# Kernel optimization log

Measured on AMD Instinct MI355X. Metric: run time of the kernel, lower is better.

## Reference

```python
import jax, jax.numpy as jnp
import numpy as np

B, S, D, F, E, K, H = 4, 1024, 512, 2048, 8, 2, 8
HEAD_DIM = D // H


def setup_inputs() -> dict:
    key = jax.random.key(0)
    ks = jax.random.split(key, 8)
    s = 0.02
    return {
        "x": jax.random.normal(ks[0], (B, S, D), jnp.float32),
        "gate_Wk": jax.random.normal(ks[1], (D, D), jnp.float32) * s,
        "gate_bk": jnp.zeros((D,), jnp.float32),
        "expert_queries": jax.random.normal(ks[2], (E, D), jnp.float32),
        "Wqkv": jax.random.normal(ks[3], (E, 3 * D, D), jnp.float32) * s,
        "bqkv": jnp.zeros((E, 3 * D), jnp.float32),
        "Wo": jax.random.normal(ks[4], (E, D, D), jnp.float32) * s,
        "bo": jnp.zeros((E, D), jnp.float32),
        "g1": jnp.ones((E, D), jnp.float32),
        "be1": jnp.zeros((E, D), jnp.float32),
        "W1": jax.random.normal(ks[5], (E, F, D), jnp.float32) * s,
        "bf1": jnp.zeros((E, F), jnp.float32),
        "W2": jax.random.normal(ks[6], (E, D, F), jnp.float32) * s,
        "bf2": jnp.zeros((E, D), jnp.float32),
        "g2": jnp.ones((E, D), jnp.float32),
        "be2": jnp.zeros((E, D), jnp.float32),
    }


def _layernorm(x, g, b):
    m = x.mean(-1, keepdims=True)
    v = ((x - m) ** 2).mean(-1, keepdims=True)
    return (x - m) * jax.lax.rsqrt(v + 1e-5) * g + b


def _expert(x, Wqkv, bqkv, Wo, bo, g1, be1, W1, bf1, W2, bf2, g2, be2):
    # x: [B,S,D]; one ExpertTransformerDecoder block (dropout=0, eval)
    b, s, d = x.shape
    qkv = x @ Wqkv.T + bqkv                      # [B,S,3D]
    q, k, v = jnp.split(qkv, 3, axis=-1)
    to_heads = lambda t: t.reshape(b, s, H, HEAD_DIM).transpose(0, 2, 1, 3)
    q, k, v = to_heads(q), to_heads(k), to_heads(v)
    scale = 1.0 / np.sqrt(HEAD_DIM).astype(np.float32)
    attn = jax.nn.softmax(jnp.einsum('bhqd,bhkd->bhqk', q * scale, k), axis=-1)
    ctx = jnp.einsum('bhqk,bhkd->bhqd', attn, v).transpose(0, 2, 1, 3).reshape(b, s, d)
    ctx = ctx @ Wo.T + bo
    x = _layernorm(x + ctx, g1, be1)
    h = jax.nn.gelu(x @ W1.T + bf1, approximate=False)
    h = jax.nn.gelu(h @ W2.T + bf2, approximate=False)
    return _layernorm(x + h, g2, be2)


def reference(x, gate_Wk, gate_bk, expert_queries, Wqkv, bqkv, Wo, bo,
              g1, be1, W1, bf1, W2, bf2, g2, be2):
    # attention gating: softmax over experts of <key_proj(x), expert_q> * d^-0.5
    keys = x @ gate_Wk.T + gate_bk                      # [B,S,D]
    scores = jnp.einsum('bsd,ed->bse', keys, expert_queries) * (D ** -0.5)
    probs = jax.nn.softmax(scores, axis=-1)             # [B,S,E]
    # top-k mask + renormalize
    _, idx = jax.lax.top_k(probs, K)                    # [B,S,K]
    mask = jax.nn.one_hot(idx, E, dtype=probs.dtype).sum(-2)
    gated = probs * mask
    gated = gated / (gated.sum(-1, keepdims=True) + 1e-9)
    # run all experts densely (as the torch code does), vmapped over E
    eo = jax.vmap(_expert, in_axes=(None,) + (0,) * 12)(
        x, Wqkv, bqkv, Wo, bo, g1, be1, W1, bf1, W2, bf2, g2, be2)  # [E,B,S,D]
    return jnp.einsum('ebsd,bse->bsd', eo, gated)
```

## Files before the change

### kernel.cpp

```cpp
#include <hip/hip_runtime.h>
#include <cstdint>
#include <cmath>

#define Bc 4
#define Sc 1024
#define Dc 512
#define Fc 2048
#define Ec 8
#define Hc 8
#define Mc 4096

typedef unsigned short u16;
typedef __attribute__((ext_vector_type(8))) short bf16x8;
typedef __attribute__((ext_vector_type(4))) float f32x4;

__device__ __forceinline__ float bf2f(u16 u) {
  unsigned v = ((unsigned)u) << 16;
  return __builtin_bit_cast(float, v);
}
__device__ __forceinline__ u16 f2bf(float f) {
  unsigned u = __builtin_bit_cast(unsigned, f);
  unsigned r = 0x7fffu + ((u >> 16) & 1u);
  return (u16)((u + r) >> 16);
}
__device__ __forceinline__ unsigned pack2bf(float a, float b) {
  return (unsigned)f2bf(a) | ((unsigned)f2bf(b) << 16);
}
__device__ __forceinline__ float gelu_f(float x) {
  const float z = 1.5957691216057308f * fmaf(0.044715f * x, x * x, x);
  const float e = __expf(z);
  return x * (1.0f - __builtin_amdgcn_rcpf(e + 1.0f));
}
__device__ __forceinline__ void async16(const void* g, void* l) {
  __builtin_amdgcn_global_load_lds(
      (const __attribute__((address_space(1))) unsigned int*)g,
      (__attribute__((address_space(3))) unsigned int*)l, 16, 0, 0);
}

__global__ __launch_bounds__(256) void cvt_kernel(const float* __restrict__ in,
                                                  u16* __restrict__ outp, long long n) {
  const long long i = ((long long)blockIdx.x * 256 + threadIdx.x) * 4;
  if (i < n) {
    const float4 v = *(const float4*)(in + i);
    ushort4 o;
    o.x = f2bf(v.x); o.y = f2bf(v.y); o.z = f2bf(v.z); o.w = f2bf(v.w);
    *(ushort4*)(outp + i) = o;
  }
}

__global__ __launch_bounds__(256) void weq_kernel(const float* __restrict__ gWk,
                                                  const float* __restrict__ eq,
                                                  float* __restrict__ weq) {
  __shared__ float red[4][64];
  const int tid = threadIdx.x, wave = tid >> 6, lane = tid & 63;
  const int d = blockIdx.x * 64 + lane;
  const int e = blockIdx.y;
  float acc = 0.f;
  for (int j = wave * 128; j < wave * 128 + 128; ++j)
    acc += gWk[(long long)j * 512 + d] * eq[e * 512 + j];
  red[wave][lane] = acc;
  __syncthreads();
  if (wave == 0)
    weq[e * 512 + d] = red[0][lane] + red[1][lane] + red[2][lane] + red[3][lane];
}
__global__ void beq_kernel(const float* __restrict__ gbk, const float* __restrict__ eq,
                           float* __restrict__ beq) {
  const int wave = threadIdx.x >> 6, lane = threadIdx.x & 63;
  for (int e = wave; e < 8; e += 4) {
    float a = 0.f;
#pragma unroll
    for (int i = 0; i < 8; ++i) a += gbk[lane + 64 * i] * eq[e * 512 + lane + 64 * i];
#pragma unroll
    for (int off = 32; off; off >>= 1) a += __shfl_xor(a, off);
    if (lane == 0) beq[e] = a;
  }
}

__global__ __launch_bounds__(256) void gate_kernel(const float* __restrict__ x,
                                                   const float* __restrict__ weq,
                                                   const float* __restrict__ beq,
                                                   float* __restrict__ gated,
                                                   int* __restrict__ cnt, int* __restrict__ tlist,
                                                   int* __restrict__ pos) {
  const int wave = threadIdx.x >> 6, lane = threadIdx.x & 63;
  const int t = blockIdx.x * 4 + wave;
  const float* xr = x + (long long)t * 512;
  float acc[8] = {};
#pragma unroll
  for (int i = 0; i < 8; ++i) {
    const float xv = xr[lane + 64 * i];
#pragma unroll
    for (int e2 = 0; e2 < 8; ++e2) acc[e2] += xv * weq[e2 * 512 + lane + 64 * i];
  }
#pragma unroll
  for (int e2 = 0; e2 < 8; ++e2)
#pragma unroll
    for (int off = 32; off; off >>= 1) acc[e2] += __shfl_xor(acc[e2], off);
  if (lane == 0) {
    const float scale = 0.044194173824159216f;
    float s[8], mx = -1e30f;
#pragma unroll
    for (int e2 = 0; e2 < 8; ++e2) { s[e2] = (acc[e2] + beq[e2]) * scale; mx = fmaxf(mx, s[e2]); }
    float p[8], sum = 0.f;
#pragma unroll
    for (int e2 = 0; e2 < 8; ++e2) { p[e2] = expf(s[e2] - mx); sum += p[e2]; }
#pragma unroll
    for (int e2 = 0; e2 < 8; ++e2) p[e2] /= sum;
    int i1 = 0;
#pragma unroll
    for (int e2 = 1; e2 < 8; ++e2) if (p[e2] > p[i1]) i1 = e2;
    int i2 = (i1 == 0) ? 1 : 0;
#pragma unroll
    for (int e2 = 0; e2 < 8; ++e2) if (e2 != i1 && e2 != i2 && p[e2] > p[i2]) i2 = e2;
    const float denom = p[i1] + p[i2] + 1e-9f;
#pragma unroll
    for (int e2 = 0; e2 < 8; ++e2)
      gated[t * 8 + e2] = (e2 == i1 || e2 == i2) ? p[e2] / denom : 0.f;
    const int b = t >> 10;
    int s1 = atomicAdd(cnt + i1 * 4 + b, 1);
    tlist[(i1 * 4 + b) * 1024 + s1] = t;
    pos[i1 * 4096 + t] = s1;
    int s2 = atomicAdd(cnt + i2 * 4 + b, 1);
    tlist[(i2 * 4 + b) * 1024 + s2] = t;
    pos[i2 * 4096 + t] = s2;
  }
}

__global__ void pad_kernel(const int* __restrict__ cnt, int* __restrict__ tlist) {
  const int seg = blockIdx.x;
  const int c = cnt[seg];
  const int ce = (c + 127) & ~127;
  const int tpad = (seg & 3) << 10;
  for (int i = c + (int)threadIdx.x; i < ce; i += 128) tlist[seg * 1024 + i] = tpad;
}

__global__ void wl_kernel(const int* __restrict__ cnt, int* __restrict__ wl) {
  const int seg = threadIdx.x;
  if (seg >= 32) return;
  int base = 0;
  for (int s = 0; s < seg; ++s) base += (cnt[s] + 127) >> 7;
  const int nt = (cnt[seg] + 127) >> 7;
  for (int t = 0; t < nt; ++t) wl[base + t] = (seg << 8) | t;
  for (int t = 0; t < 2 * nt; ++t) wl[128 + 2 * base + t] = (seg << 8) | t;
  if (seg == 31) { wl[96] = base + nt; wl[97] = 2 * (base + nt); }
}

template <int GELU, int QKV, int ROUTED, int BK>
__global__ __launch_bounds__(256) void gemm_bf16(
    const u16* __restrict__ A, const u16* __restrict__ Bw, const float* __restrict__ bias,
    u16* __restrict__ Cout, u16* __restrict__ vT, int M, int N, int K, long long Astride,
    const int* __restrict__ wl) {
  int e;
  long long bm;
  if (ROUTED) {
    const int total = wl[96];
    if ((int)blockIdx.x >= total) return;
    const int item = wl[blockIdx.x];
    const int seg = item >> 8, tile = item & 255;
    e = seg >> 2;
    bm = ((long long)(seg & 3) << 10) + tile * 128;
  } else {
    e = blockIdx.z;
    bm = (long long)blockIdx.x * 128;
  }
  __shared__ __attribute__((aligned(16))) u16 As[128 * BK];
  __shared__ __attribute__((aligned(16))) u16 Bs[128 * BK];
  const int tid = threadIdx.x;
  const int wave = tid >> 6, lane = tid & 63;
  const long long bn = (long long)blockIdx.y * 128;
  const u16* Ag = A + (long long)e * Astride + bm * K;
  const u16* Bg = Bw + ((long long)e * N + bn) * K;
  constexpr int LPR = BK / 8;
  constexpr int RPI = 512 / BK;
  constexpr int IPW = BK / 16;
  const int lrow = lane / LPR, lpos = lane % LPR;
  const int lm = lane & 15, quad = lane >> 4;
  const int wm = (wave >> 1) * 64, wn = (wave & 1) * 64;
  f32x4 acc[4][4] = {};
  for (int kk = 0; kk < K; kk += BK) {
    __syncthreads();
#pragma unroll
    for (int i = 0; i < IPW; ++i) {
      const int gi = wave * IPW + i;
      const int row = gi * RPI + lrow;
      const int sc = lpos ^ (row & 7);
      async16(Ag + (long long)row * K + kk + sc * 8, &As[gi * 512]);
      async16(Bg + (long long)row * K + kk + sc * 8, &Bs[gi * 512]);
    }
    __syncthreads();
#pragma unroll
    for (int ks = 0; ks < BK / 32; ++ks) {
      bf16x8 af[4], bfr[4];
#pragma unroll
      for (int mi = 0; mi < 4; ++mi) {
        const int row = wm + mi * 16 + lm;
        const int ch = (ks * 4 + quad) ^ (row & 7);
        af[mi] = *(const bf16x8*)(As + row * BK + ch * 8);
      }
#pragma unroll
      for (int nj = 0; nj < 4; ++nj) {
        const int row = wn + nj * 16 + lm;
        const int ch = (ks * 4 + quad) ^ (row & 7);
        bfr[nj] = *(const bf16x8*)(Bs + row * BK + ch * 8);
      }
#pragma unroll
      for (int mi = 0; mi < 4; ++mi)
#pragma unroll
        for (int nj = 0; nj < 4; ++nj)
          acc[mi][nj] = __builtin_amdgcn_mfma_f32_16x16x32_bf16(bfr[nj], af[mi], acc[mi][nj], 0, 0, 0);
    }
  }
  const float* bs = bias + (long long)e * N;
#pragma unroll
  for (int mi = 0; mi < 4; ++mi) {
    const int m = (int)bm + wm + mi * 16 + lm;
#pragma unroll
    for (int nj = 0; nj < 4; ++nj) {
      const int n0 = (int)bn + wn + nj * 16 + quad * 4;
      const float4 bv = *(const float4*)(bs + n0);
      float v0 = acc[mi][nj][0] + bv.x;
      float v1 = acc[mi][nj][1] + bv.y;
      float v2 = acc[mi][nj][2] + bv.z;
      float v3 = acc[mi][nj][3] + bv.w;
      if (GELU) { v0 = gelu_f(v0); v1 = gelu_f(v1); v2 = gelu_f(v2); v3 = gelu_f(v3); }
      if (QKV) {
        if (n0 < 1024) {
          uint2 pk; pk.x = pack2bf(v0, v1); pk.y = pack2bf(v2, v3);
          *(uint2*)(Cout + ((long long)e * Mc + m) * 1024 + n0) = pk;
        } else {
          const int hh = (n0 - 1024) >> 6, dd = (n0 - 1024) & 63;
          const int bb = m >> 10, ss = m & 1023;
          u16* vp = vT + ((((long long)e * Bc + bb) * Hc + hh) * 64 + dd) * Sc + ss;
          vp[0] = f2bf(v0); vp[Sc] = f2bf(v1); vp[2 * Sc] = f2bf(v2); vp[3 * Sc] = f2bf(v3);
        }
      } else {
        uint2 pk; pk.x = pack2bf(v0, v1); pk.y = pack2bf(v2, v3);
        *(uint2*)(Cout + ((long long)e * M + m) * N + n0) = pk;
      }
    }
  }
}

__global__ __launch_bounds__(256, 4) void attn_tile(const u16* __restrict__ qk,
                                                    const u16* __restrict__ vT,
                                                    u16* __restrict__ ctx,
                                                    const int* __restrict__ wl,
                                                    const int* __restrict__ tlist) {
  if ((int)blockIdx.x >= wl[97]) return;
  const int item = wl[128 + blockIdx.x];
  const int seg = item >> 8, qt = item & 255;
  const int e = seg >> 2, b = seg & 3, h = blockIdx.y;
  __shared__ __attribute__((aligned(16))) u16 Ks[64 * 64];
  __shared__ __attribute__((aligned(16))) u16 Vs[64 * 64];
  __shared__ __attribute__((aligned(16))) u16 Pl[4][16 * 72];
  const int tid = threadIdx.x, wave = tid >> 6, lane = tid & 63;
  const int lm = lane & 15, quad = lane >> 4;
  const u16* qkbase = qk + (long long)e * Mc * 1024;
  const u16* vbase = vT + ((((long long)e * Bc + b) * Hc + h) * 64) * Sc;
  const int lr = lane >> 3, lc = (lane & 7) ^ lr;
  u16* P = &Pl[wave][0];
  unsigned* P32 = (unsigned*)P;
  const int pwbase = lm * 36 + quad * 2;

  const long long pidx = (long long)seg * 1024 + qt * 64 + wave * 16 + lm;
  const int tq = tlist[pidx];
  bf16x8 aq[2];
#pragma unroll
  for (int ks = 0; ks < 2; ++ks)
    aq[ks] = *(const bf16x8*)(qkbase + (long long)tq * 1024 + h * 64 + ks * 32 + quad * 8);
  f32x4 O[4] = {};
  float lsum = 0.f;

  for (int n0 = 0; n0 < Sc; n0 += 64) {
    __syncthreads();
#pragma unroll
    for (int i = 0; i < 2; ++i) {
      const int rg = wave * 2 + i;
      const int row = rg * 8 + lr;
      async16(qkbase + ((long long)b * Sc + n0 + row) * 1024 + 512 + h * 64 + lc * 8,
              &Ks[rg * 512]);
      async16(vbase + (long long)row * Sc + n0 + lc * 8, &Vs[rg * 512]);
    }
    __syncthreads();
    f32x4 sT[4];
#pragma unroll
    for (int kj = 0; kj < 4; ++kj) {
      const int row = kj * 16 + lm;
      const bf16x8 k0 = *(const bf16x8*)(Ks + row * 64 + ((quad) ^ (row & 7)) * 8);
      const bf16x8 k1 = *(const bf16x8*)(Ks + row * 64 + ((4 + quad) ^ (row & 7)) * 8);
      f32x4 c = {};
      c = __builtin_amdgcn_mfma_f32_16x16x32_bf16(k0, aq[0], c, 0, 0, 0);
      c = __builtin_amdgcn_mfma_f32_16x16x32_bf16(k1, aq[1], c, 0, 0, 0);
      sT[kj] = c;
    }
#pragma unroll
    for (int kj = 0; kj < 4; ++kj) {
      const float p0 = __expf(sT[kj][0] * 0.125f);
      const float p1 = __expf(sT[kj][1] * 0.125f);
      const float p2 = __expf(sT[kj][2] * 0.125f);
      const float p3 = __expf(sT[kj][3] * 0.125f);
      lsum += (p0 + p1) + (p2 + p3);
      P32[pwbase + kj * 8 + 0] = pack2bf(p0, p1);
      P32[pwbase + kj * 8 + 1] = pack2bf(p2, p3);
    }
    asm volatile("s_waitcnt lgkmcnt(0)" ::: "memory");
    const bf16x8 ap0 = *(const bf16x8*)(P + lm * 72 + quad * 8);
    const bf16x8 ap1 = *(const bf16x8*)(P + lm * 72 + 32 + quad * 8);
#pragma unroll
    for (int d4 = 0; d4 < 4; ++d4) {
      const int row = d4 * 16 + lm;
      const bf16x8 v0 = *(const bf16x8*)(Vs + row * 64 + ((quad) ^ (row & 7)) * 8);
      const bf16x8 v1 = *(const bf16x8*)(Vs + row * 64 + ((4 + quad) ^ (row & 7)) * 8);
      O[d4] = __builtin_amdgcn_mfma_f32_16x16x32_bf16(v0, ap0, O[d4], 0, 0, 0);
      O[d4] = __builtin_amdgcn_mfma_f32_16x16x32_bf16(v1, ap1, O[d4], 0, 0, 0);
    }
  }
  float ls = lsum;
  ls += __shfl_xor(ls, 16);
  ls += __shfl_xor(ls, 32);
  const float inv = 1.0f / ls;
#pragma unroll
  for (int d4 = 0; d4 < 4; ++d4) {
    uint2 pk;
    pk.x = pack2bf(O[d4][0] * inv, O[d4][1] * inv);
    pk.y = pack2bf(O[d4][2] * inv, O[d4][3] * inv);
    *(uint2*)(ctx + pidx * 512 + h * 64 + d4 * 16 + quad * 4) = pk;
  }
}

__global__ __launch_bounds__(256) void ln1_kernel(const float* __restrict__ x,
                                                  const u16* __restrict__ ctxp,
                                                  const float* __restrict__ g1,
                                                  const float* __restrict__ be1,
                                                  u16* __restrict__ x1,
                                                  const int* __restrict__ cnt,
                                                  const int* __restrict__ tlist) {
  const int i = blockIdx.x, b = blockIdx.y, e = blockIdx.z;
  const int seg = (e << 2) + b;
  const int ce = (cnt[seg] + 127) & ~127;
  if (i >= ce) return;
  const long long p = seg * 1024 + i;
  const int t = tlist[p];
  const int tid = threadIdx.x;
  const int wave = tid >> 6, lane = tid & 63;
  __shared__ float sred[4], qred[4];
  const float v0 = x[(long long)t * 512 + tid] + bf2f(ctxp[p * 512 + tid]);
  const float v1 = x[(long long)t * 512 + tid + 256] + bf2f(ctxp[p * 512 + tid + 256]);
  float s = v0 + v1, q = v0 * v0 + v1 * v1;
#pragma unroll
  for (int off = 32; off; off >>= 1) { s += __shfl_xor(s, off); q += __shfl_xor(q, off); }
  if (lane == 0) { sred[wave] = s; qred[wave] = q; }
  __syncthreads();
  s = sred[0] + sred[1] + sred[2] + sred[3];
  q = qred[0] + qred[1] + qred[2] + qred[3];
  const float mean = s * (1.0f / 512.0f);
  const float var = q * (1.0f / 512.0f) - mean * mean;
  const float rstd = rsqrtf(var + 1e-5f);
  x1[p * 512 + tid] = f2bf((v0 - mean) * rstd * g1[e * 512 + tid] + be1[e * 512 + tid]);
  x1[p * 512 + tid + 256] =
      f2bf((v1 - mean) * rstd * g1[e * 512 + tid + 256] + be1[e * 512 + tid + 256]);
}

__global__ __launch_bounds__(256) void ln2_kernel(const u16* __restrict__ x1,
                                                  const u16* __restrict__ h2,
                                                  const float* __restrict__ g2,
                                                  const float* __restrict__ be2,
                                                  const float* __restrict__ gated,
                                                  const int* __restrict__ pos,
                                                  float* __restrict__ out) {
  const int t = blockIdx.x, tid = threadIdx.x;
  const int b = t >> 10;
  const int wave = tid >> 6, lane = tid & 63;
  __shared__ float sred[4], qred[4];
  float o0 = 0.f, o1 = 0.f;
  for (int e = 0; e < 8; ++e) {
    const float wgt = gated[t * 8 + e];
    if (wgt != 0.f) {
      const long long p = ((e << 2) + b) * 1024 + pos[e * 4096 + t];
      const float v0 = bf2f(x1[p * 512 + tid]) + bf2f(h2[p * 512 + tid]);
      const float v1 = bf2f(x1[p * 512 + tid + 256]) + bf2f(h2[p * 512 + tid + 256]);
      float s = v0 + v1, q = v0 * v0 + v1 * v1;
#pragma unroll
      for (int off = 32; off; off >>= 1) { s += __shfl_xor(s, off); q += __shfl_xor(q, off); }
      if (lane == 0) { sred[wave] = s; qred[wave] = q; }
      __syncthreads();
      s = sred[0] + sred[1] + sred[2] + sred[3];
      q = qred[0] + qred[1] + qred[2] + qred[3];
      __syncthreads();
      const float mean = s * (1.0f / 512.0f);
      const float var = q * (1.0f / 512.0f) - mean * mean;
      const float rstd = rsqrtf(var + 1e-5f);
      o0 += wgt * ((v0 - mean) * rstd * g2[e * 512 + tid] + be2[e * 512 + tid]);
      o1 += wgt * ((v1 - mean) * rstd * g2[e * 512 + tid + 256] + be2[e * 512 + tid + 256]);
    }
  }
  out[(long long)t * 512 + tid] = o0;
  out[(long long)t * 512 + tid + 256] = o1;
}

extern "C" void kernel_launch(void* const* d_in, const int* in_sizes, int n_in, void* d_out,
                              int out_size, void* d_ws, size_t ws_size, hipStream_t stream) {
  const float* x    = (const float*)d_in[0];
  const float* gWk  = (const float*)d_in[1];
  const float* gbk  = (const float*)d_in[2];
  const float* eq   = (const float*)d_in[3];
  const float* Wqkv = (const float*)d_in[4];
  const float* bqkv = (const float*)d_in[5];
  const float* Wo   = (const float*)d_in[6];
  const float* bo   = (const float*)d_in[7];
  const float* g1   = (const float*)d_in[8];
  const float* be1  = (const float*)d_in[9];
  const float* W1   = (const float*)d_in[10];
  const float* bf1  = (const float*)d_in[11];
  const float* W2   = (const float*)d_in[12];
  const float* bf2  = (const float*)d_in[13];
  const float* g2   = (const float*)d_in[14];
  const float* be2  = (const float*)d_in[15];
  float* out = (float*)d_out;

  char* wsp = (char*)d_ws;
  size_t off = 0;
  auto take = [&](size_t bytes) -> void* {
    void* p = wsp + off;
    off += (bytes + 255) & ~(size_t)255;
    return p;
  };
  u16* xb    = (u16*)take((size_t)Mc * 512 * 2);
  u16* Wqkvb = (u16*)take((size_t)Ec * 1536 * 512 * 2);
  u16* Wob   = (u16*)take((size_t)Ec * 512 * 512 * 2);
  u16* W1b   = (u16*)take((size_t)Ec * 2048 * 512 * 2);
  u16* W2b   = (u16*)take((size_t)Ec * 512 * 2048 * 2);
  float* weq   = (float*)take(8 * 512 * 4);
  float* beqb  = (float*)take(8 * 4);
  float* gated = (float*)take((size_t)Mc * 8 * 4);
  int* cnt   = (int*)take(32 * 4);
  int* tlist = (int*)take(32 * 1024 * 4);
  int* pos   = (int*)take((size_t)Ec * Mc * 4);
  int* wl    = (int*)take(512 * 4);
  char* big = (char*)take(134217728);
  u16* qkb  = (u16*)big;
  u16* vTb  = (u16*)(big + 67108864);
  u16* ctxp = (u16*)(big + 100663296);
  u16* hb   = (u16*)big;
  u16* ctxb = (u16*)take(33554432);
  u16* h2b  = ctxb;
  u16* x1b  = (u16*)take(33554432);
  (void)in_sizes; (void)n_in; (void)out_size; (void)ws_size;

  cvt_kernel<<<dim3(2048), dim3(256), 0, stream>>>(x, xb, (long long)Mc * 512);
  cvt_kernel<<<dim3(6144), dim3(256), 0, stream>>>(Wqkv, Wqkvb, (long long)Ec * 1536 * 512);
  cvt_kernel<<<dim3(2048), dim3(256), 0, stream>>>(Wo, Wob, (long long)Ec * 512 * 512);
  cvt_kernel<<<dim3(8192), dim3(256), 0, stream>>>(W1, W1b, (long long)Ec * 2048 * 512);
  cvt_kernel<<<dim3(8192), dim3(256), 0, stream>>>(W2, W2b, (long long)Ec * 512 * 2048);
  hipMemsetAsync(cnt, 0, 32 * 4, stream);
  weq_kernel<<<dim3(8, 8), dim3(256), 0, stream>>>(gWk, eq, weq);
  beq_kernel<<<dim3(1), dim3(256), 0, stream>>>(gbk, eq, beqb);
  gate_kernel<<<dim3(1024), dim3(256), 0, stream>>>(x, weq, beqb, gated, cnt, tlist, pos);
  pad_kernel<<<dim3(32), dim3(128), 0, stream>>>(cnt, tlist);
  wl_kernel<<<dim3(1), dim3(64), 0, stream>>>(cnt, wl);
  gemm_bf16<0, 1, 0, 64><<<dim3(32, 12, 8), dim3(256), 0, stream>>>(xb, Wqkvb, bqkv, qkb, vTb, Mc, 1536, 512, 0LL, wl);
  attn_tile<<<dim3(192, 8), dim3(256), 0, stream>>>(qkb, vTb, ctxb, wl, tlist);
  gemm_bf16<0, 0, 1, 128><<<dim3(96, 4), dim3(256), 0, stream>>>(ctxb, Wob, bo, ctxp, nullptr, Mc, 512, 512, (long long)Mc * 512, wl);
  ln1_kernel<<<dim3(1024, 4, 8), dim3(256), 0, stream>>>(x, ctxp, g1, be1, x1b, cnt, tlist);
  gemm_bf16<1, 0, 1, 128><<<dim3(96, 16), dim3(256), 0, stream>>>(x1b, W1b, bf1, hb, nullptr, Mc, 2048, 512, (long long)Mc * 512, wl);
  gemm_bf16<1, 0, 1, 128><<<dim3(96, 4), dim3(256), 0, stream>>>(hb, W2b, bf2, h2b, nullptr, Mc, 512, 2048, (long long)Mc * 2048, wl);
  ln2_kernel<<<dim3(4096), dim3(256), 0, stream>>>(x1b, h2b, g2, be2, gated, pos, out);
}
```

Measured before the change: 509.7 us.

## Compute Q projection only for routed tokens via gathered GEMM; fuse weight conversions

The dense QKV GEMM now computes only K and V for every token. Q is computed by a separate routed GEMM that gathers A rows through the token list, so it covers only the tokens assigned to each expert. The attention kernel reads Q directly by routed position and reads K from its own buffer, with no tlist indirection. The five fp32-to-bf16 conversion launches are merged into one kernel. The intent is to skip Q projection work for unrouted tokens and to cut launch overhead, at the cost of gathered, less coalesced A loads in the Q GEMM.

```diff
diff --git a/kernel.cpp b/kernel.cpp
--- a/kernel.cpp
+++ b/kernel.cpp
@@ -37,15 +37,24 @@
       (__attribute__((address_space(3))) unsigned int*)l, 16, 0, 0);
 }
 
-__global__ __launch_bounds__(256) void cvt_kernel(const float* __restrict__ in,
-                                                  u16* __restrict__ outp, long long n) {
-  const long long i = ((long long)blockIdx.x * 256 + threadIdx.x) * 4;
-  if (i < n) {
-    const float4 v = *(const float4*)(in + i);
-    ushort4 o;
-    o.x = f2bf(v.x); o.y = f2bf(v.y); o.z = f2bf(v.z); o.w = f2bf(v.w);
-    *(ushort4*)(outp + i) = o;
-  }
+__global__ __launch_bounds__(256) void cvt5_kernel(const float* __restrict__ p0, u16* __restrict__ q0,
+                                                   const float* __restrict__ p1, u16* __restrict__ q1,
+                                                   const float* __restrict__ p2, u16* __restrict__ q2,
+                                                   const float* __restrict__ p3, u16* __restrict__ q3,
+                                                   const float* __restrict__ p4, u16* __restrict__ q4) {
+  int bx = blockIdx.x;
+  const float* in;
+  u16* outp;
+  if (bx < 2048) { in = p0; outp = q0; }
+  else if (bx < 8192) { in = p1; outp = q1; bx -= 2048; }
+  else if (bx < 10240) { in = p2; outp = q2; bx -= 8192; }
+  else if (bx < 18432) { in = p3; outp = q3; bx -= 10240; }
+  else { in = p4; outp = q4; bx -= 18432; }
+  const long long i = ((long long)bx * 256 + threadIdx.x) * 4;
+  const float4 v = *(const float4*)(in + i);
+  ushort4 o;
+  o.x = f2bf(v.x); o.y = f2bf(v.y); o.z = f2bf(v.z); o.w = f2bf(v.w);
+  *(ushort4*)(outp + i) = o;
 }
 
 __global__ __launch_bounds__(256) void weq_kernel(const float* __restrict__ gWk,
@@ -145,11 +154,11 @@
   if (seg == 31) { wl[96] = base + nt; wl[97] = 2 * (base + nt); }
 }
 
-template <int GELU, int QKV, int ROUTED, int BK>
+template <int GELU, int QKV, int ROUTED, int BK, int GATHER>
 __global__ __launch_bounds__(256) void gemm_bf16(
     const u16* __restrict__ A, const u16* __restrict__ Bw, const float* __restrict__ bias,
     u16* __restrict__ Cout, u16* __restrict__ vT, int M, int N, int K, long long Astride,
-    const int* __restrict__ wl) {
+    long long Bstride, const int* __restrict__ wl, const int* __restrict__ tlist) {
   int e;
   long long bm;
   if (ROUTED) {
@@ -169,13 +178,22 @@
   const int wave = tid >> 6, lane = tid & 63;
   const long long bn = (long long)blockIdx.y * 128;
   const u16* Ag = A + (long long)e * Astride + bm * K;
-  const u16* Bg = Bw + ((long long)e * N + bn) * K;
+  const u16* Bg = Bw + ((long long)e * Bstride + bn) * K;
   constexpr int LPR = BK / 8;
   constexpr int RPI = 512 / BK;
   constexpr int IPW = BK / 16;
   const int lrow = lane / LPR, lpos = lane % LPR;
   const int lm = lane & 15, quad = lane >> 4;
   const int wm = (wave >> 1) * 64, wn = (wave & 1) * 64;
+  int tok[IPW];
+  if (GATHER) {
+    const long long tbase = (long long)e * 4096 + bm;
+#pragma unroll
+    for (int i = 0; i < IPW; ++i) {
+      const int gi = wave * IPW + i;
+      tok[i] = tlist[tbase + gi * RPI + lrow];
+    }
+  }
   f32x4 acc[4][4] = {};
   for (int kk = 0; kk < K; kk += BK) {
     __syncthreads();
@@ -184,7 +202,10 @@
       const int gi = wave * IPW + i;
       const int row = gi * RPI + lrow;
       const int sc = lpos ^ (row & 7);
-      async16(Ag + (long long)row * K + kk + sc * 8, &As[gi * 512]);
+      if (GATHER)
+        async16(A + (long long)tok[i] * K + kk + sc * 8, &As[gi * 512]);
+      else
+        async16(Ag + (long long)row * K + kk + sc * 8, &As[gi * 512]);
       async16(Bg + (long long)row * K + kk + sc * 8, &Bs[gi * 512]);
     }
     __syncthreads();
@@ -210,7 +231,7 @@
           acc[mi][nj] = __builtin_amdgcn_mfma_f32_16x16x32_bf16(bfr[nj], af[mi], acc[mi][nj], 0, 0, 0);
     }
   }
-  const float* bs = bias + (long long)e * N;
+  const float* bs = bias + (long long)e * Bstride;
 #pragma unroll
   for (int mi = 0; mi < 4; ++mi) {
     const int m = (int)bm + wm + mi * 16 + lm;
@@ -224,11 +245,11 @@
       float v3 = acc[mi][nj][3] + bv.w;
       if (GELU) { v0 = gelu_f(v0); v1 = gelu_f(v1); v2 = gelu_f(v2); v3 = gelu_f(v3); }
       if (QKV) {
-        if (n0 < 1024) {
+        if (n0 < 512) {
           uint2 pk; pk.x = pack2bf(v0, v1); pk.y = pack2bf(v2, v3);
-          *(uint2*)(Cout + ((long long)e * Mc + m) * 1024 + n0) = pk;
+          *(uint2*)(Cout + ((long long)e * Mc + m) * 512 + n0) = pk;
         } else {
-          const int hh = (n0 - 1024) >> 6, dd = (n0 - 1024) & 63;
+          const int hh = (n0 - 512) >> 6, dd = (n0 - 512) & 63;
           const int bb = m >> 10, ss = m & 1023;
           u16* vp = vT + ((((long long)e * Bc + bb) * Hc + hh) * 64 + dd) * Sc + ss;
           vp[0] = f2bf(v0); vp[Sc] = f2bf(v1); vp[2 * Sc] = f2bf(v2); vp[3 * Sc] = f2bf(v3);
@@ -241,11 +262,11 @@
   }
 }
 
-__global__ __launch_bounds__(256, 4) void attn_tile(const u16* __restrict__ qk,
+__global__ __launch_bounds__(256, 4) void attn_tile(const u16* __restrict__ qb,
+                                                    const u16* __restrict__ kb,
                                                     const u16* __restrict__ vT,
                                                     u16* __restrict__ ctx,
-                                                    const int* __restrict__ wl,
-                                                    const int* __restrict__ tlist) {
+                                                    const int* __restrict__ wl) {
   if ((int)blockIdx.x >= wl[97]) return;
   const int item = wl[128 + blockIdx.x];
   const int seg = item >> 8, qt = item & 255;
@@ -255,7 +276,7 @@
   __shared__ __attribute__((aligned(16))) u16 Pl[4][16 * 72];
   const int tid = threadIdx.x, wave = tid >> 6, lane = tid & 63;
   const int lm = lane & 15, quad = lane >> 4;
-  const u16* qkbase = qk + (long long)e * Mc * 1024;
+  const u16* kbase = kb + ((long long)e * Mc + b * Sc) * 512;
   const u16* vbase = vT + ((((long long)e * Bc + b) * Hc + h) * 64) * Sc;
   const int lr = lane >> 3, lc = (lane & 7) ^ lr;
   u16* P = &Pl[wave][0];
@@ -263,11 +284,10 @@
   const int pwbase = lm * 36 + quad * 2;
 
   const long long pidx = (long long)seg * 1024 + qt * 64 + wave * 16 + lm;
-  const int tq = tlist[pidx];
   bf16x8 aq[2];
 #pragma unroll
   for (int ks = 0; ks < 2; ++ks)
-    aq[ks] = *(const bf16x8*)(qkbase + (long long)tq * 1024 + h * 64 + ks * 32 + quad * 8);
+    aq[ks] = *(const bf16x8*)(qb + pidx * 512 + h * 64 + ks * 32 + quad * 8);
   f32x4 O[4] = {};
   float lsum = 0.f;
 
@@ -277,8 +297,7 @@
     for (int i = 0; i < 2; ++i) {
       const int rg = wave * 2 + i;
       const int row = rg * 8 + lr;
-      async16(qkbase + ((long long)b * Sc + n0 + row) * 1024 + 512 + h * 64 + lc * 8,
-              &Ks[rg * 512]);
+      async16(kbase + (long long)(n0 + row) * 512 + h * 64 + lc * 8, &Ks[rg * 512]);
       async16(vbase + (long long)row * Sc + n0 + lc * 8, &Vs[rg * 512]);
     }
     __syncthreads();
@@ -438,7 +457,8 @@
   int* pos   = (int*)take((size_t)Ec * Mc * 4);
   int* wl    = (int*)take(512 * 4);
   char* big = (char*)take(134217728);
-  u16* qkb  = (u16*)big;
+  u16* qb   = (u16*)big;
+  u16* kb   = (u16*)(big + 33554432);
   u16* vTb  = (u16*)(big + 67108864);
   u16* ctxp = (u16*)(big + 100663296);
   u16* hb   = (u16*)big;
@@ -447,22 +467,24 @@
   u16* x1b  = (u16*)take(33554432);
   (void)in_sizes; (void)n_in; (void)out_size; (void)ws_size;
 
-  cvt_kernel<<<dim3(2048), dim3(256), 0, stream>>>(x, xb, (long long)Mc * 512);
-  cvt_kernel<<<dim3(6144), dim3(256), 0, stream>>>(Wqkv, Wqkvb, (long long)Ec * 1536 * 512);
-  cvt_kernel<<<dim3(2048), dim3(256), 0, stream>>>(Wo, Wob, (long long)Ec * 512 * 512);
-  cvt_kernel<<<dim3(8192), dim3(256), 0, stream>>>(W1, W1b, (long long)Ec * 2048 * 512);
-  cvt_kernel<<<dim3(8192), dim3(256), 0, stream>>>(W2, W2b, (long long)Ec * 512 * 2048);
+  cvt5_kernel<<<dim3(26624), dim3(256), 0, stream>>>(x, xb, Wqkv, Wqkvb, Wo, Wob, W1, W1b, W2, W2b);
   hipMemsetAsync(cnt, 0, 32 * 4, stream);
   weq_kernel<<<dim3(8, 8), dim3(256), 0, stream>>>(gWk, eq, weq);
   beq_kernel<<<dim3(1), dim3(256), 0, stream>>>(gbk, eq, beqb);
   gate_kernel<<<dim3(1024), dim3(256), 0, stream>>>(x, weq, beqb, gated, cnt, tlist, pos);
   pad_kernel<<<dim3(32), dim3(128), 0, stream>>>(cnt, tlist);
   wl_kernel<<<dim3(1), dim3(64), 0, stream>>>(cnt, wl);
-  gemm_bf16<0, 1, 0, 64><<<dim3(32, 12, 8), dim3(256), 0, stream>>>(xb, Wqkvb, bqkv, qkb, vTb, Mc, 1536, 512, 0LL, wl);
-  attn_tile<<<dim3(192, 8), dim3(256), 0, stream>>>(qkb, vTb, ctxb, wl, tlist);
-  gemm_bf16<0, 0, 1, 128><<<dim3(96, 4), dim3(256), 0, stream>>>(ctxb, Wob, bo, ctxp, nullptr, Mc, 512, 512, (long long)Mc * 512, wl);
+  gemm_bf16<0, 1, 0, 64, 0><<<dim3(32, 8, 8), dim3(256), 0, stream>>>(
+      xb, Wqkvb + 512 * 512, bqkv + 512, kb, vTb, Mc, 1024, 512, 0LL, 1536LL, wl, nullptr);
+  gemm_bf16<0, 0, 1, 128, 1><<<dim3(96, 4), dim3(256), 0, stream>>>(
+      xb, Wqkvb, bqkv, qb, nullptr, Mc, 512, 512, 0LL, 1536LL, wl, tlist);
+  attn_tile<<<dim3(192, 8), dim3(256), 0, stream>>>(qb, kb, vTb, ctxb, wl);
+  gemm_bf16<0, 0, 1, 128, 0><<<dim3(96, 4), dim3(256), 0, stream>>>(
+      ctxb, Wob, bo, ctxp, nullptr, Mc, 512, 512, (long long)Mc * 512, 512LL, wl, nullptr);
   ln1_kernel<<<dim3(1024, 4, 8), dim3(256), 0, stream>>>(x, ctxp, g1, be1, x1b, cnt, tlist);
-  gemm_bf16<1, 0, 1, 128><<<dim3(96, 16), dim3(256), 0, stream>>>(x1b, W1b, bf1, hb, nullptr, Mc, 2048, 512, (long long)Mc * 512, wl);
-  gemm_bf16<1, 0, 1, 128><<<dim3(96, 4), dim3(256), 0, stream>>>(hb, W2b, bf2, h2b, nullptr, Mc, 512, 2048, (long long)Mc * 2048, wl);
+  gemm_bf16<1, 0, 1, 128, 0><<<dim3(96, 16), dim3(256), 0, stream>>>(
+      x1b, W1b, bf1, hb, nullptr, Mc, 2048, 512, (long long)Mc * 512, 2048LL, wl, nullptr);
+  gemm_bf16<1, 0, 1, 128, 0><<<dim3(96, 4), dim3(256), 0, stream>>>(
+      hb, W2b, bf2, h2b, nullptr, Mc, 512, 2048, (long long)Mc * 2048, 512LL, wl, nullptr);
   ln2_kernel<<<dim3(4096), dim3(256), 0, stream>>>(x1b, h2b, g2, be2, gated, pos, out);
 }
```

Measured after the change: 481.8 us. -5.5%, faster.
